# Kernel optimization log

Hardware: AMD Instinct MI355X
Metric: run time of the kernel (lower is better)

The kernel has to match this reference:

```python
import jax, jax.numpy as jnp
import numpy as np

N_NODES = 100000

def gcn_conv(x, src, dst, W, b, n):
    # PyG GCNConv: h = W x; add self-loops; norm = d^-1/2[src] * d^-1/2[dst]; scatter-add at dst; + b
    h = x @ W
    loop = jnp.arange(n, dtype=src.dtype)
    s = jnp.concatenate([src, loop])
    d = jnp.concatenate([dst, loop])
    deg = jax.ops.segment_sum(jnp.ones_like(d, dtype=h.dtype), d, num_segments=n)
    dis = jnp.where(deg > 0, jax.lax.rsqrt(deg), 0.0)
    norm = dis[s] * dis[d]                     # [E+n]
    msg = h[s] * norm[:, None]                  # [E+n, F] big gather
    out = jax.ops.segment_sum(msg, d, num_segments=n)
    return out + b

def setup_inputs() -> dict:
    key = jax.random.key(0)
    ks = jax.random.split(key, 12)
    n, e, f = N_NODES, 3200000, 14
    hid = [64, 64, 32]
    c = 2
    x = jax.random.normal(ks[0], (n, f), dtype=jnp.float32)
    edge_index = jax.random.randint(ks[1], (2, e), 0, n, dtype=jnp.int64)
    batch = jnp.sort(jax.random.randint(ks[2], (n,), 0, 2000, dtype=jnp.int64))
    def lin(k, fi, fo):
        s = 1.0 / np.sqrt(fi)
        return jax.random.uniform(k, (fi, fo), jnp.float32, -s, s)
    W1 = lin(ks[3], f, hid[0]); b1 = jnp.zeros((hid[0],), jnp.float32)
    W2 = lin(ks[4], hid[0], hid[1]); b2 = jnp.zeros((hid[1],), jnp.float32)
    W3 = lin(ks[5], hid[1], hid[2]); b3 = jnp.zeros((hid[2],), jnp.float32)
    W4 = lin(ks[6], hid[2], c); b4 = jnp.zeros((c,), jnp.float32)
    return {"x": x, "edge_index": edge_index, "batch": batch, "num_graphs": 2000,
            "W1": W1, "b1": b1, "W2": W2, "b2": b2, "W3": W3, "b3": b3, "W4": W4, "b4": b4}

def reference(x, edge_index, batch, num_graphs, W1, b1, W2, b2, W3, b3, W4, b4):
    n = x.shape[0]
    src, dst = edge_index[0], edge_index[1]
    h = jax.nn.relu(gcn_conv(x, src, dst, W1, b1, n))   # dropout = identity at inference
    h = jax.nn.relu(gcn_conv(h, src, dst, W2, b2, n))
    h = jax.nn.relu(gcn_conv(h, src, dst, W3, b3, n))
    h = gcn_conv(h, src, dst, W4, b4, n)
    # global mean pool over graphs
    sums = jax.ops.segment_sum(h, batch, num_segments=num_graphs)
    cnts = jax.ops.segment_sum(jnp.ones((n,), h.dtype), batch, num_segments=num_graphs)
    pooled = sums / jnp.maximum(cnts, 1.0)[:, None]
    return jax.nn.log_softmax(pooled, axis=-1)
```

## Files before the change

### kernel.cpp

```cpp
#include <hip/hip_runtime.h>
#include <hip/hip_fp16.h>
#include <math.h>
#include <type_traits>

static constexpr int THREADS = 256;
static constexpr int CAP   = 80;
static constexpr int BSH   = 9;
static constexpr int SUBS  = 4;
static constexpr int SUBN  = 128;
static constexpr int CAPB  = 17920;
static constexpr int MAXB  = 256;
static constexpr int L4WN  = 256;

typedef float v2f __attribute__((ext_vector_type(2)));


__global__ __launch_bounds__(THREADS)
void k_part(const int* __restrict__ src, const int* __restrict__ dst,
            int* __restrict__ bcnt, int* __restrict__ pairs, int e, int nbuck) {
    __shared__ int hist[MAXB];
    __shared__ int base_s[MAXB];
    for (int i = threadIdx.x; i < nbuck; i += THREADS) hist[i] = 0;
    __syncthreads();

    int i0 = (blockIdx.x * THREADS + (int)threadIdx.x) * 8;
    int ss[8], dd[8], bb[8], rk[8];
    int c8 = 0;
    if (i0 < e) {
        c8 = min(8, e - i0);
        if (c8 == 8) {
            int4 d0 = ((const int4*)(dst + i0))[0];
            int4 d1 = ((const int4*)(dst + i0))[1];
            int4 s0 = ((const int4*)(src + i0))[0];
            int4 s1 = ((const int4*)(src + i0))[1];
            dd[0]=d0.x; dd[1]=d0.y; dd[2]=d0.z; dd[3]=d0.w;
            dd[4]=d1.x; dd[5]=d1.y; dd[6]=d1.z; dd[7]=d1.w;
            ss[0]=s0.x; ss[1]=s0.y; ss[2]=s0.z; ss[3]=s0.w;
            ss[4]=s1.x; ss[5]=s1.y; ss[6]=s1.z; ss[7]=s1.w;
        } else {
            for (int j = 0; j < c8; ++j) { dd[j] = dst[i0 + j]; ss[j] = src[i0 + j]; }
        }
        for (int j = 0; j < c8; ++j) {
            bb[j] = dd[j] >> BSH;
            rk[j] = atomicAdd(&hist[bb[j]], 1);
        }
    }
    __syncthreads();
    for (int i = threadIdx.x; i < nbuck; i += THREADS)
        base_s[i] = hist[i] ? atomicAdd(&bcnt[i], hist[i]) : 0;
    __syncthreads();
    for (int j = 0; j < c8; ++j) {
        int idx = base_s[bb[j]] + rk[j];
        if (idx < CAPB)
            pairs[(size_t)bb[j] * CAPB + idx] = ((dd[j] & ((1 << BSH) - 1)) << 17) | ss[j];
    }
}


__global__ __launch_bounds__(THREADS)
void k_scat2(const int* __restrict__ pairs, const int* __restrict__ bcnt,
             const float* __restrict__ x, int* __restrict__ cnt, int* __restrict__ csr,
             float* __restrict__ dis, __half2* __restrict__ xs, int n) {
    __shared__ int slab[SUBN * CAP];
    __shared__ int lcnt[SUBN];
    int bucket = blockIdx.x / SUBS;
    int sub    = blockIdx.x % SUBS;
    int gnode0 = (bucket << BSH) + sub * SUBN;
    if (gnode0 >= n) return;
    for (int i = threadIdx.x; i < SUBN; i += THREADS) lcnt[i] = 0;
    __syncthreads();

    int m = min(bcnt[bucket], CAPB);
    const int* pp = pairs + (size_t)bucket * CAPB;
    for (int i0 = (int)threadIdx.x * 4; i0 < m; i0 += THREADS * 4) {
        int k = min(4, m - i0);
        int v[4];
        if (k == 4) {
            int4 a = *(const int4*)(pp + i0);
            v[0] = a.x; v[1] = a.y; v[2] = a.z; v[3] = a.w;
        } else {
            for (int j = 0; j < k; ++j) v[j] = pp[i0 + j];
        }
#pragma unroll
        for (int j = 0; j < 4; ++j) {
            if (j < k) {
                int dl = v[j] >> 17;
                if ((dl >> 7) == sub) {
                    int ln = dl & (SUBN - 1);
                    int p = atomicAdd(&lcnt[ln], 1);
                    if (p < CAP) slab[ln * CAP + p] = v[j] & 0x1FFFF;
                }
            }
        }
    }
    __syncthreads();

    size_t gbase = (size_t)gnode0 * CAP;
    for (int idx = threadIdx.x; idx < SUBN * CAP; idx += THREADS) {
        int node = gnode0 + idx / CAP;
        if (node < n) csr[gbase + idx] = slab[idx];
    }
    if (threadIdx.x < SUBN) {
        int node = gnode0 + (int)threadIdx.x;
        if (node < n) {
            int dg = min(lcnt[threadIdx.x], CAP);
            cnt[node] = dg;
            float dn = rsqrtf((float)(dg + 1));
            dis[node] = dn;
            const float* xr = x + (size_t)node * 14;
            __half2* o = xs + (size_t)node * 8;
#pragma unroll
            for (int fl = 0; fl < 7; ++fl) {
                float2 v;
                v.x = dn * xr[fl * 2];
                v.y = dn * xr[fl * 2 + 1];
                o[fl] = __float22half2_rn(v);
            }
            o[7] = __float22half2_rn(make_float2(0.f, 0.f));
        }
    }
}


__global__ __launch_bounds__(THREADS)
void k_gather_l1(const __half2* __restrict__ hw, const int* __restrict__ deg,
                 const int* __restrict__ csr, const float* __restrict__ dis,
                 float* __restrict__ out, int n) {
    constexpr int SG = 4, HPL = 2, RS = 8;
    int tid = blockIdx.x * THREADS + threadIdx.x;
    int node = tid / SG;
    int fl = tid % SG;
    if (node >= n) return;
    size_t o = (size_t)node * CAP;
    int dg = deg[node];
    float dn = dis[node];

    auto loadrow = [&](int s, __half2* r) {
        union { uint2 u; __half2 h[2]; } t;
        t.u = *(const uint2*)(hw + (size_t)s * RS + fl * HPL);
        r[0] = t.h[0]; r[1] = t.h[1];
    };

    float2 self[HPL];
    {
        __half2 r[HPL];
        loadrow(node, r);
#pragma unroll
        for (int q = 0; q < HPL; ++q) {
            self[q] = __half22float2(r[q]);
            self[q].x *= dn; self[q].y *= dn;
        }
    }

    __half2 z = __float2half2_rn(0.f);
    __half2 c0[HPL], c1[HPL], c2[HPL], c3[HPL];
#pragma unroll
    for (int q = 0; q < HPL; ++q) { c0[q] = z; c1[q] = z; c2[q] = z; c3[q] = z; }

    int base = 0;
    for (; base + SG <= dg; base += SG) {
        int cs = csr[o + base + fl];
#pragma unroll
        for (int t = 0; t < SG; t += 4) {
            int s0 = __shfl(cs, t, SG),     s1 = __shfl(cs, t + 1, SG);
            int s2 = __shfl(cs, t + 2, SG), s3 = __shfl(cs, t + 3, SG);
            __half2 r0[HPL], r1[HPL], r2[HPL], r3[HPL];
            loadrow(s0, r0); loadrow(s1, r1); loadrow(s2, r2); loadrow(s3, r3);
#pragma unroll
            for (int q = 0; q < HPL; ++q) {
                c0[q] = __hadd2(c0[q], r0[q]);
                c1[q] = __hadd2(c1[q], r1[q]);
                c2[q] = __hadd2(c2[q], r2[q]);
                c3[q] = __hadd2(c3[q], r3[q]);
            }
        }
    }
    int rem = dg - base;
    if (rem > 0) {
        int cs = (fl < rem) ? csr[o + base + fl] : 0;
        for (int t = 0; t < rem; ++t) {
            int s = __shfl(cs, t, SG);
            __half2 r[HPL];
            loadrow(s, r);
#pragma unroll
            for (int q = 0; q < HPL; ++q) c0[q] = __hadd2(c0[q], r[q]);
        }
    }

    float* op = out + (size_t)node * 2 * RS + fl * 2 * HPL;
#pragma unroll
    for (int q = 0; q < HPL; ++q) {
        float2 v0 = __half22float2(c0[q]), v1 = __half22float2(c1[q]);
        float2 v2 = __half22float2(c2[q]), v3 = __half22float2(c3[q]);
        op[q * 2 + 0] = self[q].x + (v0.x + v1.x) + (v2.x + v3.x);
        op[q * 2 + 1] = self[q].y + (v0.y + v1.y) + (v2.y + v3.y);
    }
}


template<int SG>
__global__ __launch_bounds__(THREADS)
void k_gather_f8(const unsigned char* __restrict__ hw, const int* __restrict__ deg,
                 const int* __restrict__ csr, const float* __restrict__ dis,
                 const float* __restrict__ bias, __half* __restrict__ out, int n) {
    constexpr int RSB = SG * 8;
    int tid = blockIdx.x * THREADS + threadIdx.x;
    int node = tid / SG;
    int fl = tid % SG;
    if (node >= n) return;
    size_t o = (size_t)node * CAP;
    int dg = deg[node];
    float dn = dis[node];

    auto loadrow = [&](int s, v2f* r) {
        uint2 u = *(const uint2*)(hw + (size_t)s * RSB + fl * 8);
        r[0] = __builtin_amdgcn_cvt_pk_f32_fp8(u.x, false);
        r[1] = __builtin_amdgcn_cvt_pk_f32_fp8(u.x, true);
        r[2] = __builtin_amdgcn_cvt_pk_f32_fp8(u.y, false);
        r[3] = __builtin_amdgcn_cvt_pk_f32_fp8(u.y, true);
    };

    v2f self[4];
    loadrow(node, self);

    v2f c0[4], c1[4], c2[4], c3[4];
#pragma unroll
    for (int q = 0; q < 4; ++q) { c0[q] = 0.f; c1[q] = 0.f; c2[q] = 0.f; c3[q] = 0.f; }

    int base = 0;
    for (; base + SG <= dg; base += SG) {
        int cs = csr[o + base + fl];
#pragma unroll
        for (int t = 0; t < SG; t += 4) {
            int s0 = __shfl(cs, t, SG),     s1 = __shfl(cs, t + 1, SG);
            int s2 = __shfl(cs, t + 2, SG), s3 = __shfl(cs, t + 3, SG);
            v2f r0[4], r1[4], r2[4], r3[4];
            loadrow(s0, r0); loadrow(s1, r1); loadrow(s2, r2); loadrow(s3, r3);
#pragma unroll
            for (int q = 0; q < 4; ++q) {
                c0[q] += r0[q]; c1[q] += r1[q]; c2[q] += r2[q]; c3[q] += r3[q];
            }
        }
    }
    int rem = dg - base;
    if (rem > 0) {
        int cs = (fl < rem) ? csr[o + base + fl] : 0;
        for (int t = 0; t < rem; ++t) {
            int s = __shfl(cs, t, SG);
            v2f r[4];
            loadrow(s, r);
#pragma unroll
            for (int q = 0; q < 4; ++q) c0[q] += r[q];
        }
    }

    __half* op = out + (size_t)node * SG * 8 + fl * 8;
    union { __half2 h[4]; uint4 u; } p;
#pragma unroll
    for (int q = 0; q < 4; ++q) {
        v2f v = self[q] + (c0[q] + c1[q]) + (c2[q] + c3[q]);
        v *= dn;
        float2 b = ((const float2*)bias)[fl * 4 + q];
        float vx = fmaxf(v.x + b.x, 0.f);
        float vy = fmaxf(v.y + b.y, 0.f);
        p.h[q] = __floats2half2_rn(vx, vy);
    }
    *(uint4*)op = p.u;
}


__global__ __launch_bounds__(THREADS)
void k_gather_l3(const unsigned char* __restrict__ hw, const int* __restrict__ deg,
                 const int* __restrict__ csr, const float* __restrict__ dis,
                 const float* __restrict__ b3, const float* __restrict__ W4,
                 float2* __restrict__ hw4, int n) {
    constexpr int SG = 4, RSB = 32;
    __shared__ float Ws4[64];
    if (threadIdx.x < 64) Ws4[threadIdx.x] = W4[threadIdx.x];
    __syncthreads();

    int tid = blockIdx.x * THREADS + threadIdx.x;
    int node = tid / SG;
    int fl = tid % SG;
    if (node >= n) return;
    size_t o = (size_t)node * CAP;
    int dg = deg[node];
    float dn = dis[node];

    auto loadrow = [&](int s, v2f* r) {
        uint2 u = *(const uint2*)(hw + (size_t)s * RSB + fl * 8);
        r[0] = __builtin_amdgcn_cvt_pk_f32_fp8(u.x, false);
        r[1] = __builtin_amdgcn_cvt_pk_f32_fp8(u.x, true);
        r[2] = __builtin_amdgcn_cvt_pk_f32_fp8(u.y, false);
        r[3] = __builtin_amdgcn_cvt_pk_f32_fp8(u.y, true);
    };

    v2f self[4];
    loadrow(node, self);

    v2f c0[4], c1[4], c2[4], c3[4];
#pragma unroll
    for (int q = 0; q < 4; ++q) { c0[q] = 0.f; c1[q] = 0.f; c2[q] = 0.f; c3[q] = 0.f; }

    int base = 0;
    for (; base + SG <= dg; base += SG) {
        int cs = csr[o + base + fl];
#pragma unroll
        for (int t = 0; t < SG; t += 4) {
            int s0 = __shfl(cs, t, SG),     s1 = __shfl(cs, t + 1, SG);
            int s2 = __shfl(cs, t + 2, SG), s3 = __shfl(cs, t + 3, SG);
            v2f r0[4], r1[4], r2[4], r3[4];
            loadrow(s0, r0); loadrow(s1, r1); loadrow(s2, r2); loadrow(s3, r3);
#pragma unroll
            for (int q = 0; q < 4; ++q) {
                c0[q] += r0[q]; c1[q] += r1[q]; c2[q] += r2[q]; c3[q] += r3[q];
            }
        }
    }
    int rem = dg - base;
    if (rem > 0) {
        int cs = (fl < rem) ? csr[o + base + fl] : 0;
        for (int t = 0; t < rem; ++t) {
            int s = __shfl(cs, t, SG);
            v2f r[4];
            loadrow(s, r);
#pragma unroll
            for (int q = 0; q < 4; ++q) c0[q] += r[q];
        }
    }

    float p0 = 0.f, p1 = 0.f;
#pragma unroll
    for (int q = 0; q < 4; ++q) {
        v2f v = self[q] + (c0[q] + c1[q]) + (c2[q] + c3[q]);
        v *= dn;
        float2 b = ((const float2*)b3)[fl * 4 + q];
        float vx = fmaxf(v.x + b.x, 0.f);
        float vy = fmaxf(v.y + b.y, 0.f);
        int f = 8 * fl + 2 * q;
        p0 += vx * Ws4[f * 2 + 0] + vy * Ws4[(f + 1) * 2 + 0];
        p1 += vx * Ws4[f * 2 + 1] + vy * Ws4[(f + 1) * 2 + 1];
    }
    p0 += __shfl_xor(p0, 1, SG); p0 += __shfl_xor(p0, 2, SG);
    p1 += __shfl_xor(p1, 1, SG); p1 += __shfl_xor(p1, 2, SG);
    if (fl == 0) hw4[node] = make_float2(p0 * dn, p1 * dn);
}


__global__ __launch_bounds__(THREADS)
void k_l4pool(const int* __restrict__ pairs, const int* __restrict__ bcnt,
              const float2* __restrict__ hw4, const float* __restrict__ dis,
              const float* __restrict__ b4, const int* __restrict__ batch,
              float* __restrict__ sums, float* __restrict__ cnts, int n) {
    __shared__ float accx[L4WN], accy[L4WN];
    int bucket = blockIdx.x >> 1;
    int sub    = blockIdx.x & 1;
    int gnode0 = (bucket << BSH) + sub * L4WN;
    if (gnode0 >= n) return;
    for (int i = threadIdx.x; i < L4WN; i += THREADS) { accx[i] = 0.f; accy[i] = 0.f; }
    __syncthreads();

    int m = min(bcnt[bucket], CAPB);
    const int* pp = pairs + (size_t)bucket * CAPB;
    for (int i0 = (int)threadIdx.x * 4; i0 < m; i0 += THREADS * 4) {
        int k = min(4, m - i0);
        int v[4];
        if (k == 4) {
            int4 a = *(const int4*)(pp + i0);
            v[0] = a.x; v[1] = a.y; v[2] = a.z; v[3] = a.w;
        } else {
            for (int j = 0; j < k; ++j) v[j] = pp[i0 + j];
        }
        float2 w[4]; int ln[4]; bool ok[4];
#pragma unroll
        for (int j = 0; j < 4; ++j) {
            int dl = v[j] >> 17;
            ok[j] = (j < k) && ((dl >> 8) == sub);
            ln[j] = dl & (L4WN - 1);
            int s = ok[j] ? (v[j] & 0x1FFFF) : 0;
            w[j] = hw4[s];
        }
#pragma unroll
        for (int j = 0; j < 4; ++j) {
            if (ok[j]) {
                atomicAdd(&accx[ln[j]], w[j].x);
                atomicAdd(&accy[ln[j]], w[j].y);
            }
        }
    }
    __syncthreads();

    if (threadIdx.x < L4WN / 8) {
        int i0 = threadIdx.x * 8;
        int nvalid = min(gnode0 + L4WN, n) - gnode0;
        int end = min(i0 + 8, nvalid);
        if (i0 < nvalid) {
            float bx = b4[0], by = b4[1];
            int g = batch[gnode0 + i0];
            float v0 = 0.f, v1 = 0.f, c = 0.f;
            for (int i = i0; i < end; ++i) {
                int node = gnode0 + i;
                int gi = batch[node];
                if (gi != g) {
                    atomicAdd(&sums[g * 2 + 0], v0);
                    atomicAdd(&sums[g * 2 + 1], v1);
                    atomicAdd(&cnts[g], c);
                    g = gi; v0 = 0.f; v1 = 0.f; c = 0.f;
                }
                float2 self = hw4[node];
                float dn = dis[node];
                v0 += (self.x + accx[i]) * dn + bx;
                v1 += (self.y + accy[i]) * dn + by;
                c += 1.0f;
            }
            atomicAdd(&sums[g * 2 + 0], v0);
            atomicAdd(&sums[g * 2 + 1], v1);
            atomicAdd(&cnts[g], c);
        }
    }
}

__global__ void k_logsoftmax(const float* __restrict__ sums, const float* __restrict__ cnts,
                             float* __restrict__ out, int ng) {
    int g = blockIdx.x * blockDim.x + threadIdx.x;
    if (g >= ng) return;
    float c = fmaxf(cnts[g], 1.0f);
    float p0 = sums[g * 2 + 0] / c;
    float p1 = sums[g * 2 + 1] / c;
    float m = fmaxf(p0, p1);
    float l = m + logf(expf(p0 - m) + expf(p1 - m));
    out[g * 2 + 0] = p0 - l;
    out[g * 2 + 1] = p1 - l;
}


template<int KW, int K, int KSTR, int FOUT, bool EPI_BIAS_RELU, int OUTM, typename IN_T>
__global__ __launch_bounds__(THREADS)
void k_gemm_rb(const IN_T* __restrict__ in, const float* __restrict__ W,
               const float* __restrict__ dis, const float* __restrict__ bias,
               void* __restrict__ outv, int n) {
    constexpr int CG = FOUT / 4;
    constexpr bool IN_HALF = std::is_same<IN_T, __half>::value;
    constexpr int CH = IN_HALF ? 8 : 4;
    __shared__ float Ws[K * FOUT];
    for (int i = threadIdx.x; i < K * FOUT; i += THREADS) {
        int r = i / FOUT;
        Ws[i] = (r < KW) ? W[i] : 0.0f;
    }
    __syncthreads();
    int gid = blockIdx.x * THREADS + threadIdx.x;
    int pair = gid / CG, cg = gid % CG;
    int node0 = pair * 2;
    if (node0 >= n) return;
    bool two = (node0 + 1 < n);
    const IN_T* r0 = in + (size_t)node0 * KSTR;
    const IN_T* r1 = two ? in + (size_t)(node0 + 1) * KSTR : r0;
    const float4* Wf4 = (const float4*)Ws;
    float4 acc0 = {0.f, 0.f, 0.f, 0.f}, acc1 = {0.f, 0.f, 0.f, 0.f};
#pragma unroll
    for (int k0 = 0; k0 < K / CH; ++k0) {
        float xv0[CH], xv1[CH];
        if constexpr (IN_HALF) {
            union { uint4 u; __half2 h[4]; } t0, t1;
            t0.u = ((const uint4*)r0)[k0];
            t1.u = ((const uint4*)r1)[k0];
#pragma unroll
            for (int i = 0; i < 4; ++i) {
                float2 g0 = __half22float2(t0.h[i]);
                float2 g1 = __half22float2(t1.h[i]);
                xv0[2 * i] = g0.x; xv0[2 * i + 1] = g0.y;
                xv1[2 * i] = g1.x; xv1[2 * i + 1] = g1.y;
            }
        } else {
            float4 a0 = ((const float4*)r0)[k0];
            float4 a1 = ((const float4*)r1)[k0];
#pragma unroll
            for (int i = 0; i < 4; ++i) { xv0[i] = (&a0.x)[i]; xv1[i] = (&a1.x)[i]; }
        }
#pragma unroll
        for (int kk = 0; kk < CH; ++kk) {
            float4 wv = Wf4[(k0 * CH + kk) * CG + cg];
            float a = xv0[kk], b = xv1[kk];
            acc0.x += a * wv.x; acc0.y += a * wv.y; acc0.z += a * wv.z; acc0.w += a * wv.w;
            acc1.x += b * wv.x; acc1.y += b * wv.y; acc1.z += b * wv.z; acc1.w += b * wv.w;
        }
    }
    float dn0 = dis[node0];
    float dn1 = two ? dis[node0 + 1] : 0.f;
    acc0.x *= dn0; acc0.y *= dn0; acc0.z *= dn0; acc0.w *= dn0;
    acc1.x *= dn1; acc1.y *= dn1; acc1.z *= dn1; acc1.w *= dn1;
    if (EPI_BIAS_RELU) {
        float4 bv = ((const float4*)bias)[cg];
        acc0.x = fmaxf(acc0.x + bv.x, 0.f); acc0.y = fmaxf(acc0.y + bv.y, 0.f);
        acc0.z = fmaxf(acc0.z + bv.z, 0.f); acc0.w = fmaxf(acc0.w + bv.w, 0.f);
        acc1.x = fmaxf(acc1.x + bv.x, 0.f); acc1.y = fmaxf(acc1.y + bv.y, 0.f);
        acc1.z = fmaxf(acc1.z + bv.z, 0.f); acc1.w = fmaxf(acc1.w + bv.w, 0.f);
    }
    if constexpr (OUTM == 2) {
        unsigned char* ob = (unsigned char*)outv;
        int w0 = 0;
        w0 = __builtin_amdgcn_cvt_pk_fp8_f32(acc0.x, acc0.y, w0, false);
        w0 = __builtin_amdgcn_cvt_pk_fp8_f32(acc0.z, acc0.w, w0, true);
        *(unsigned*)(ob + (size_t)node0 * FOUT + cg * 4) = (unsigned)w0;
        if (two) {
            int w1 = 0;
            w1 = __builtin_amdgcn_cvt_pk_fp8_f32(acc1.x, acc1.y, w1, false);
            w1 = __builtin_amdgcn_cvt_pk_fp8_f32(acc1.z, acc1.w, w1, true);
            *(unsigned*)(ob + (size_t)(node0 + 1) * FOUT + cg * 4) = (unsigned)w1;
        }
    } else if constexpr (OUTM == 1) {
        __half* out = (__half*)outv;
        union { __half2 h[2]; uint2 u; } p0, p1;
        p0.h[0] = __floats2half2_rn(acc0.x, acc0.y);
        p0.h[1] = __floats2half2_rn(acc0.z, acc0.w);
        *(uint2*)(out + (size_t)node0 * FOUT + cg * 4) = p0.u;
        if (two) {
            p1.h[0] = __floats2half2_rn(acc1.x, acc1.y);
            p1.h[1] = __floats2half2_rn(acc1.z, acc1.w);
            *(uint2*)(out + (size_t)(node0 + 1) * FOUT + cg * 4) = p1.u;
        }
    } else {
        float* out = (float*)outv;
        ((float4*)(out + (size_t)node0 * FOUT))[cg] = acc0;
        if (two) ((float4*)(out + (size_t)(node0 + 1) * FOUT))[cg] = acc1;
    }
}


static inline int nblk(long long t) { return (int)((t + THREADS - 1) / THREADS); }

extern "C" void kernel_launch(void* const* d_in, const int* in_sizes, int n_in,
                              void* d_out, int out_size, void* d_ws, size_t ws_size,
                              hipStream_t stream) {
    const float* x     = (const float*)d_in[0];
    const int*   ei    = (const int*)d_in[1];
    const int*   batch = (const int*)d_in[2];
    const float* W1 = (const float*)d_in[4];
    const float* b1 = (const float*)d_in[5];
    const float* W2 = (const float*)d_in[6];
    const float* b2 = (const float*)d_in[7];
    const float* W3 = (const float*)d_in[8];
    const float* b3 = (const float*)d_in[9];
    const float* W4 = (const float*)d_in[10];
    const float* b4 = (const float*)d_in[11];

    const int n  = in_sizes[0] / 14;
    const int e  = in_sizes[1] / 2;
    const int ng = out_size / 2;
    const int* src = ei;
    const int* dst = ei + e;
    const int nbuck = (n + (1 << BSH) - 1) >> BSH;

    char* ws = (char*)d_ws;
    size_t off_b = 0;
    auto alloc = [&](size_t bytes) -> char* {
        char* p = ws + off_b;
        off_b = (off_b + bytes + 255) & ~(size_t)255;
        return p;
    };
    int*     cnt  = (int*)alloc((size_t)n * 4);
    char*    zbase = alloc((size_t)MAXB * 4);
    int*     bcnt = (int*)zbase;
    float*   sums = (float*)alloc((size_t)ng * 2 * 4);
    float*   cnts = (float*)alloc((size_t)ng * 4);
    size_t   zspan = (size_t)((char*)cnts + (size_t)ng * 4 - zbase);
    float*   dis  = (float*)alloc((size_t)n * 4);
    int*     csr  = (int*)alloc((size_t)n * CAP * 4);
    int*     pairs= (int*)alloc((size_t)nbuck * CAPB * 4);
    __half2* xs16 = (__half2*)alloc((size_t)n * 8 * 4);
    float*   agg1 = (float*)alloc((size_t)n * 16 * 4);
    __half*  hbuf16 = (__half*)alloc((size_t)n * 64 * 2);
    unsigned char* hw8 = (unsigned char*)alloc((size_t)n * 64);
    float*   hw4  = (float*)alloc((size_t)n * 2 * 4);
    (void)ws_size; (void)n_in;

    hipMemsetAsync(zbase, 0, zspan, stream);
    k_part<<<nblk(((long long)e + 7) / 8), THREADS, 0, stream>>>(src, dst, bcnt, pairs, e, nbuck);
    k_scat2<<<nbuck * SUBS, THREADS, 0, stream>>>(pairs, bcnt, x, cnt, csr, dis, xs16, n);

    k_gather_l1<<<nblk((long long)n * 4), THREADS, 0, stream>>>(
        xs16, cnt, csr, dis, agg1, n);
    k_gemm_rb<14, 16, 16, 64, true, 1, float><<<nblk((long long)(n / 2 + 1) * 16), THREADS, 0, stream>>>(
        agg1, W1, dis, b1, hbuf16, n);

    k_gemm_rb<64, 64, 64, 64, false, 2, __half><<<nblk((long long)(n / 2 + 1) * 16), THREADS, 0, stream>>>(
        hbuf16, W2, dis, nullptr, hw8, n);
    k_gather_f8<8><<<nblk((long long)n * 8), THREADS, 0, stream>>>(
        hw8, cnt, csr, dis, b2, hbuf16, n);

    k_gemm_rb<64, 64, 64, 32, false, 2, __half><<<nblk((long long)(n / 2 + 1) * 8), THREADS, 0, stream>>>(
        hbuf16, W3, dis, nullptr, hw8, n);
    k_gather_l3<<<nblk((long long)n * 4), THREADS, 0, stream>>>(
        hw8, cnt, csr, dis, b3, W4, (float2*)hw4, n);

    k_l4pool<<<nbuck * 2, THREADS, 0, stream>>>(
        pairs, bcnt, (const float2*)hw4, dis, b4, batch, sums, cnts, n);
    k_logsoftmax<<<nblk(ng), THREADS, 0, stream>>>(sums, cnts, (float*)d_out, ng);
}
```

Measured before the change: 313.6 us.

## Split layer-4 aggregation into chunked partial-sum kernel plus reduce-and-pool kernel

```diff
diff --git a/kernel.cpp b/kernel.cpp
--- a/kernel.cpp
+++ b/kernel.cpp
@@ -11,6 +11,7 @@
 static constexpr int CAPB  = 17920;
 static constexpr int MAXB  = 256;
 static constexpr int L4WN  = 256;
+static constexpr int NCH   = 8;
 
 typedef float v2f __attribute__((ext_vector_type(2)));
 
@@ -348,22 +349,24 @@
 
 
 __global__ __launch_bounds__(THREADS)
-void k_l4pool(const int* __restrict__ pairs, const int* __restrict__ bcnt,
-              const float2* __restrict__ hw4, const float* __restrict__ dis,
-              const float* __restrict__ b4, const int* __restrict__ batch,
-              float* __restrict__ sums, float* __restrict__ cnts, int n) {
+void k_l4a(const int* __restrict__ pairs, const int* __restrict__ bcnt,
+           const float2* __restrict__ hw4, float2* __restrict__ part, int n) {
     __shared__ float accx[L4WN], accy[L4WN];
-    int bucket = blockIdx.x >> 1;
-    int sub    = blockIdx.x & 1;
+    int w     = blockIdx.x / NCH;
+    int chunk = blockIdx.x % NCH;
+    int bucket = w >> 1;
+    int sub    = w & 1;
     int gnode0 = (bucket << BSH) + sub * L4WN;
     if (gnode0 >= n) return;
     for (int i = threadIdx.x; i < L4WN; i += THREADS) { accx[i] = 0.f; accy[i] = 0.f; }
     __syncthreads();
 
     int m = min(bcnt[bucket], CAPB);
+    int c0 = ((chunk * m) / NCH) & ~3;
+    int c1 = (chunk == NCH - 1) ? m : (((chunk + 1) * m) / NCH) & ~3;
     const int* pp = pairs + (size_t)bucket * CAPB;
-    for (int i0 = (int)threadIdx.x * 4; i0 < m; i0 += THREADS * 4) {
-        int k = min(4, m - i0);
+    for (int i0 = c0 + (int)threadIdx.x * 4; i0 < c1; i0 += THREADS * 4) {
+        int k = min(4, c1 - i0);
         int v[4];
         if (k == 4) {
             int4 a = *(const int4*)(pp + i0);
@@ -371,22 +374,56 @@
         } else {
             for (int j = 0; j < k; ++j) v[j] = pp[i0 + j];
         }
-        float2 w[4]; int ln[4]; bool ok[4];
+        float2 wv[4]; int ln[4]; bool ok[4];
 #pragma unroll
         for (int j = 0; j < 4; ++j) {
             int dl = v[j] >> 17;
             ok[j] = (j < k) && ((dl >> 8) == sub);
             ln[j] = dl & (L4WN - 1);
             int s = ok[j] ? (v[j] & 0x1FFFF) : 0;
-            w[j] = hw4[s];
+            wv[j] = hw4[s];
         }
 #pragma unroll
         for (int j = 0; j < 4; ++j) {
             if (ok[j]) {
-                atomicAdd(&accx[ln[j]], w[j].x);
-                atomicAdd(&accy[ln[j]], w[j].y);
-            }
-        }
+                atomicAdd(&accx[ln[j]], wv[j].x);
+                atomicAdd(&accy[ln[j]], wv[j].y);
+            }
+        }
+    }
+    __syncthreads();
+
+    float2* op = part + ((size_t)w * NCH + chunk) * L4WN;
+    for (int i = threadIdx.x; i < L4WN; i += THREADS)
+        op[i] = make_float2(accx[i], accy[i]);
+}
+
+
+__global__ __launch_bounds__(THREADS)
+void k_l4b(const float2* __restrict__ part, const float2* __restrict__ hw4,
+           const float* __restrict__ dis, const float* __restrict__ b4,
+           const int* __restrict__ batch, float* __restrict__ sums,
+           float* __restrict__ cnts, int n) {
+    __shared__ float h0s[L4WN], h1s[L4WN];
+    int w = blockIdx.x;
+    int bucket = w >> 1;
+    int sub    = w & 1;
+    int gnode0 = (bucket << BSH) + sub * L4WN;
+    if (gnode0 >= n) return;
+    int i = threadIdx.x;
+    int node = gnode0 + i;
+    if (node < n) {
+        const float2* pp = part + (size_t)w * NCH * L4WN;
+        float ax = 0.f, ay = 0.f;
+#pragma unroll
+        for (int ch = 0; ch < NCH; ++ch) {
+            float2 p = pp[ch * L4WN + i];
+            ax += p.x; ay += p.y;
+        }
+        float2 self = hw4[node];
+        float dn = dis[node];
+        h0s[i] = (self.x + ax) * dn + b4[0];
+        h1s[i] = (self.y + ay) * dn + b4[1];
     }
     __syncthreads();
 
@@ -395,22 +432,18 @@
         int nvalid = min(gnode0 + L4WN, n) - gnode0;
         int end = min(i0 + 8, nvalid);
         if (i0 < nvalid) {
-            float bx = b4[0], by = b4[1];
             int g = batch[gnode0 + i0];
             float v0 = 0.f, v1 = 0.f, c = 0.f;
-            for (int i = i0; i < end; ++i) {
-                int node = gnode0 + i;
-                int gi = batch[node];
+            for (int q = i0; q < end; ++q) {
+                int gi = batch[gnode0 + q];
                 if (gi != g) {
                     atomicAdd(&sums[g * 2 + 0], v0);
                     atomicAdd(&sums[g * 2 + 1], v1);
                     atomicAdd(&cnts[g], c);
                     g = gi; v0 = 0.f; v1 = 0.f; c = 0.f;
                 }
-                float2 self = hw4[node];
-                float dn = dis[node];
-                v0 += (self.x + accx[i]) * dn + bx;
-                v1 += (self.y + accy[i]) * dn + by;
+                v0 += h0s[q];
+                v1 += h1s[q];
                 c += 1.0f;
             }
             atomicAdd(&sums[g * 2 + 0], v0);
@@ -550,6 +583,7 @@
     const int* src = ei;
     const int* dst = ei + e;
     const int nbuck = (n + (1 << BSH) - 1) >> BSH;
+    const int nwin  = nbuck * 2;
 
     char* ws = (char*)d_ws;
     size_t off_b = 0;
@@ -572,6 +606,7 @@
     __half*  hbuf16 = (__half*)alloc((size_t)n * 64 * 2);
     unsigned char* hw8 = (unsigned char*)alloc((size_t)n * 64);
     float*   hw4  = (float*)alloc((size_t)n * 2 * 4);
+    float2*  part = (float2*)alloc((size_t)nwin * NCH * L4WN * 8);
     (void)ws_size; (void)n_in;
 
     hipMemsetAsync(zbase, 0, zspan, stream);
@@ -593,7 +628,9 @@
     k_gather_l3<<<nblk((long long)n * 4), THREADS, 0, stream>>>(
         hw8, cnt, csr, dis, b3, W4, (float2*)hw4, n);
 
-    k_l4pool<<<nbuck * 2, THREADS, 0, stream>>>(
-        pairs, bcnt, (const float2*)hw4, dis, b4, batch, sums, cnts, n);
+    k_l4a<<<nwin * NCH, THREADS, 0, stream>>>(
+        pairs, bcnt, (const float2*)hw4, part, n);
+    k_l4b<<<nwin, THREADS, 0, stream>>>(
+        part, (const float2*)hw4, dis, b4, batch, sums, cnts, n);
     k_logsoftmax<<<nblk(ng), THREADS, 0, stream>>>(sums, cnts, (float*)d_out, ng);
 }
```

New measurement: 309.5 us. No clear change (-1.3%).
